# Kernel tuning notes

Hardware: AMD Instinct MI355X
Metric: run time of the kernel (lower is better)

Reference implementation:

```python
import jax, jax.numpy as jnp
import numpy as np

BN_EPS = 1e-5


def _conv1x1(x, W, b):
    # x: (B, Cin, H, W), W: (Cout, Cin), b: (Cout,)
    return jnp.einsum('bchw,oc->bohw', x, W) + b[None, :, None, None]


def _bn(x, gamma, beta, mean, var):
    # inference-mode BatchNorm2d with running stats
    inv = gamma / jnp.sqrt(var + BN_EPS)
    return x * inv[None, :, None, None] + (beta - mean * inv)[None, :, None, None]


def setup_inputs() -> dict:
    key = jax.random.key(0)
    ks = jax.random.split(key, 8)
    B, N, C, H, W = 4, 3, 256, 48, 48
    Ck = C // 2  # key/query/value channels (scale=2)
    s = 0.02
    return {
        'x': jax.random.normal(ks[0], (B, N, C, H, W), jnp.float32),
        # f_key / f_query (shared): conv1x1 + BN
        'Wk': jax.random.normal(ks[1], (Ck, C), jnp.float32) * s,
        'bk': jnp.zeros((Ck,), jnp.float32),
        'gk': jnp.ones((Ck,), jnp.float32),
        'betak': jnp.zeros((Ck,), jnp.float32),
        'mk': jnp.zeros((Ck,), jnp.float32),
        'vk': jnp.ones((Ck,), jnp.float32),
        # f_value
        'Wv': jax.random.normal(ks[2], (Ck, C), jnp.float32) * s,
        'bv': jnp.zeros((Ck,), jnp.float32),
        # f_out
        'Wo': jax.random.normal(ks[3], (C, Ck), jnp.float32) * s,
        'bo': jnp.zeros((C,), jnp.float32),
        # fuse_layer: in = 2*C, out = C
        'Wf': jax.random.normal(ks[4], (C, 2 * C), jnp.float32) * s,
        'bf': jnp.zeros((C,), jnp.float32),
    }


def reference(x, Wk, bk, gk, betak, mk, vk, Wv, bv, Wo, bo, Wf, bf):
    B, N, C, H, W = x.shape  # N == 3
    HW = H * W
    Ck = Wk.shape[0]
    scale = Ck ** (-0.5)

    # Precompute shared key/query and value features for all 3 views
    xf = x.reshape(B * N, C, H, W)
    k_all = _bn(_conv1x1(xf, Wk, bk), gk, betak, mk, vk).reshape(B, N, Ck, HW)
    v_all = _conv1x1(xf, Wv, bv).reshape(B, N, Ck, HW)

    outs = []
    attn_maps = []
    for i in range(3):  # fixed small structural loop over views
        adj_ids = [j for j in range(3) if j != i]
        ref = x[:, i]                          # (B, C, H, W)
        q = k_all[:, i].transpose(0, 2, 1)     # (B, HW, Ck)  f_query == f_key
        matching = jnp.zeros_like(ref)
        for j in adj_ids:
            sim = jnp.einsum('bqc,bck->bqk', q, k_all[:, j]) * scale  # (B, HW, HW)
            attn = jax.nn.softmax(sim, axis=-1)
            ctx = jnp.einsum('bqk,bck->bcq', attn, v_all[:, j])       # (B, Ck, HW)
            ctx = ctx.reshape(B, Ck, H, W)
            matching = matching + _conv1x1(ctx, Wo, bo)
            if i == 0:
                attn_maps.append(attn)
        fuse = _conv1x1(jnp.concatenate([ref, matching], axis=1), Wf, bf)
        outs.append(ref + fuse)

    out = jnp.stack(outs, axis=1)                    # (B, 3, C, H, W)
    attention_maps = jnp.stack(attn_maps, axis=1)    # (B, 2, HW, HW)
    return out, attention_maps
```

## Files before the change

kernel.cpp:

```cpp
#include <hip/hip_runtime.h>

typedef short s8v __attribute__((ext_vector_type(8)));
typedef short s4v __attribute__((ext_vector_type(4)));
typedef float f4v __attribute__((ext_vector_type(4)));
typedef unsigned u32v2 __attribute__((ext_vector_type(2)));
typedef unsigned short u16;

#define MFMA(a,b,c) __builtin_amdgcn_mfma_f32_16x16x32_bf16(a,b,c,0,0,0)

__device__ __forceinline__ float bf2f(u16 x){
  unsigned u = ((unsigned)x) << 16;
  return __builtin_bit_cast(float, u);
}
__device__ __forceinline__ u16 f2bf(float f){
  unsigned u = __builtin_bit_cast(unsigned, f);
  u += 0x7FFFu + ((u >> 16) & 1u);
  return (u16)(u >> 16);
}
__device__ __forceinline__ unsigned cvtpk(float lo, float hi){
  unsigned r;
  asm("v_cvt_pk_bf16_f32 %0, %1, %2" : "=v"(r) : "v"(lo), "v"(hi));
  return r;
}

__device__ __forceinline__ void gload16(const void* g, void* l){
  __builtin_amdgcn_global_load_lds((const __attribute__((address_space(1))) unsigned*)g,
                                   (__attribute__((address_space(3))) unsigned*)l, 16, 0, 0);
}
__device__ __forceinline__ void nt_store4(float* p, f4v v){
  __builtin_nontemporal_store(v, (f4v*)p);
}

#define CC   256
#define CK   128
#define HW   2304
#define NF   12
#define C2E  0.1275174996992022f
#define OFF_KT   0u
#define OFF_V    7077888u
#define OFF_CTX  14155776u
#define OFF_RS   42467328u
#define OFF_PAR  42909696u
#define OFF_WK16 42911744u
#define OFF_WV16 42977280u
#define OFF_WF16 43042816u
#define OFF_WCMB 43304960u

__global__ void k0_params(const float* __restrict__ Wkf, const float* __restrict__ Wvf,
                          const float* __restrict__ bk, const float* __restrict__ gk,
                          const float* __restrict__ betak, const float* __restrict__ mk,
                          const float* __restrict__ vk, const float* __restrict__ Wo,
                          const float* __restrict__ Wf, const float* __restrict__ bo,
                          const float* __restrict__ bfv,
                          u16* __restrict__ Wk16, u16* __restrict__ Wv16, u16* __restrict__ Wf16,
                          float* kscale, float* kbias, float* btot, u16* Wcomb){
  int c = blockIdx.x;
  int o = threadIdx.x;
  int gid = c*256 + o;
  Wk16[gid] = f2bf(Wkf[gid]);
  Wv16[gid] = f2bf(Wvf[gid]);
  {
    f4v wf4 = *(const f4v*)(Wf + (size_t)gid*4);
    #pragma unroll
    for(int u=0;u<4;u++) Wf16[(size_t)gid*4+u] = f2bf(wf4[u]);
  }
  float acc = 0.f;
  for(int m=0;m<256;m++)
    acc += Wf[(size_t)o*512 + 256 + m] * Wo[(size_t)m*128 + c];
  Wcomb[(size_t)o*128 + c] = f2bf(acc);
  if (c == 0){
    float a2 = 0.f;
    for(int m=0;m<256;m++)
      a2 += Wf[(size_t)o*512 + 256 + m] * bo[m];
    btot[o] = bfv[o] + 2.0f*a2;
    if (o < 128){
      float inv = gk[o] * rsqrtf(vk[o] + 1e-5f);
      kscale[o] = inv;
      kbias[o]  = betak[o] + (bk[o] - mk[o])*inv;
    }
  }
}

__device__ __forceinline__ void stage_xt(const float* __restrict__ xf, int pb, int tid, char* xt){
  #pragma unroll
  for(int it=0; it<8; ++it){
    int idx = tid + 256*it;
    int cp = idx>>4, slot = idx&15;
    const float* s0 = xf + (size_t)(2*cp  )*HW + pb + slot*4;
    const float* s1 = xf + (size_t)(2*cp+1)*HW + pb + slot*4;
    f4v va = *(const f4v*)s0;
    f4v vb = *(const f4v*)s1;
    #pragma unroll
    for(int u=0;u<4;u++){
      int p = slot*4+u;
      *(unsigned*)(xt + p*512 + ((4*cp) ^ ((p&7)<<4))) = cvtpk(va[u], vb[u]);
    }
  }
}
__device__ __forceinline__ s8v xt_frag(const char* xt, int r, int kt, int g){
  return *(const s8v*)(xt + r*512 + (((unsigned)(64*kt+16*g)) ^ ((unsigned)(r&7)<<4)));
}

__global__ __launch_bounds__(256) void k1_kv(const float* __restrict__ x, const u16* __restrict__ Wk,
                                             const u16* __restrict__ Wv, const float* __restrict__ bv,
                                             const float* __restrict__ kscale, const float* __restrict__ kbias,
                                             u16* __restrict__ kT, u16* __restrict__ vout){
  int f  = blockIdx.y;
  int pb = blockIdx.x*64;
  int tid = threadIdx.x;
  int w = tid>>6, l = tid&63, s = l&15, g = l>>4;
  __shared__ char xt[32768];
  stage_xt(x + (size_t)f*CC*HW, pb, tid, xt);
  __syncthreads();
  {
    s8v afr[8];
    #pragma unroll
    for(int kt=0;kt<8;kt++) afr[kt] = xt_frag(xt, 16*w+s, kt, g);
    f4v acc[8] = {};
    #pragma unroll
    for(int kt=0;kt<8;kt++){
      #pragma unroll
      for(int nt=0;nt<8;nt++){
        s8v b = *(const s8v*)(Wk + (size_t)(16*nt+s)*CC + 32*kt + 8*g);
        acc[nt] = MFMA(afr[kt], b, acc[nt]);
      }
    }
    u16* kout = kT + (size_t)f*HW*CK;
    int q0 = pb + 16*w;
    #pragma unroll
    for(int nt=0;nt<8;nt++){
      int o = 16*nt + s;
      float sc = kscale[o], bi = kbias[o];
      #pragma unroll
      for(int r=0;r<4;r++){
        int q = q0 + 4*g + r;
        kout[(size_t)q*CK + o] = f2bf(acc[nt][r]*sc + bi);
      }
    }
  }
  {
    s8v afr[2][8];
    #pragma unroll
    for(int mt=0;mt<2;mt++)
      #pragma unroll
      for(int kt=0;kt<8;kt++)
        afr[mt][kt] = *(const s8v*)(Wv + (size_t)(32*w+16*mt+s)*CC + 32*kt + 8*g);
    f4v acc[2][4] = {};
    #pragma unroll
    for(int kt=0;kt<8;kt++){
      #pragma unroll
      for(int nt=0;nt<4;nt++){
        s8v b = xt_frag(xt, 16*nt+s, kt, g);
        #pragma unroll
        for(int mt=0;mt<2;mt++)
          acc[mt][nt] = MFMA(afr[mt][kt], b, acc[mt][nt]);
      }
    }
    u16* vf = vout + (size_t)f*CK*HW;
    #pragma unroll
    for(int mt=0;mt<2;mt++){
      #pragma unroll
      for(int r=0;r<4;r++){
        int o = 32*w + 16*mt + 4*g + r;
        float bvo = bv[o];
        #pragma unroll
        for(int nt=0;nt<4;nt++)
          vf[(size_t)o*HW + pb + 16*nt + s] = f2bf(acc[mt][nt][r] + bvo);
      }
    }
  }
}

__global__ __launch_bounds__(256, 2) void k2_attn(const u16* __restrict__ kT, const u16* __restrict__ v,
                                                  u16* __restrict__ ctxS, float* __restrict__ rs){
  int qb  = blockIdx.x;
  int yy  = blockIdx.y;
  int bij = yy>>1, half = yy&1;
  int b = bij/6, r6_ = bij - 6*b, i = r6_>>1, jj = r6_&1;
  int adj0 = (i==0) ? 1 : 0;
  int adj1 = (i==2) ? 1 : 2;
  int j = jj ? adj1 : adj0;
  int tid = threadIdx.x;
  int w = tid>>6, l = tid&63, s = l&15, g = l>>4;
  int q0 = qb*128 + w*32;

  __shared__ char L[81920];
  char* plw = L + 65536 + w*4096;

  const u16* kTi = kT + (size_t)(b*3+i)*HW*CK;
  const u16* kTj = kT + (size_t)(b*3+j)*HW*CK;
  const u16* vj  = v  + (size_t)(b*3+j)*CK*HW;

  s8v qfr[2][4];
  #pragma unroll
  for(int qf=0;qf<2;qf++)
    #pragma unroll
    for(int kt=0;kt<4;kt++)
      qfr[qf][kt] = *(const s8v*)(kTi + (size_t)(q0+16*qf+s)*CK + 32*kt + 8*g);

  f4v ctx[8][2] = {};
  float psum[2] = {0.f, 0.f};

  auto STAGE = [&](int p0, int buf){
    const char* kbase = (const char*)kTj + (size_t)p0*256;
    const char* vbase = (const char*)vj  + (size_t)p0*2;
    char* lK = L + buf*16384 + w*1024;
    char* lV = L + 32768 + buf*16384 + w*1024;
    #pragma unroll
    for(int it=0; it<4; ++it){
      unsigned Lo = (unsigned)tid*16u + (unsigned)it*4096u;
      unsigned Gs = Lo ^ (((Lo>>8)&7u)<<4);
      gload16(kbase + Gs, lK + it*4096);
      unsigned row = Lo>>7;
      unsigned col = (Lo & 127u) ^ ((row&7u)<<4);
      gload16(vbase + (size_t)row*(HW*2) + col, lV + it*4096);
    }
  };

  int pbase = half*18;
  STAGE(pbase*64, 0);
  __syncthreads();
  int cur = 0;

  for(int pt=0; pt<18; ++pt){
    int p0 = (pbase + pt)*64;
    if (pt < 17) STAGE(p0+64, cur^1);
    const char* lK = L + cur*16384;
    const char* lV = L + 32768 + cur*16384;

    f4v sa[2][4] = {};
    #pragma unroll
    for(int kt=0;kt<4;kt++){
      #pragma unroll
      for(int nt=0;nt<4;nt++){
        unsigned row = (unsigned)(16*nt + s);
        unsigned cb  = ((unsigned)(64*kt + 16*g)) ^ ((row&7u)<<4);
        s8v kfr = *(const s8v*)(lK + row*256 + cb);
        #pragma unroll
        for(int qf=0;qf<2;qf++) sa[qf][nt] = MFMA(kfr, qfr[qf][kt], sa[qf][nt]);
      }
    }
    #pragma unroll
    for(int qf=0;qf<2;qf++){
      #pragma unroll
      for(int nt=0;nt<4;nt++){
        float e0 = exp2f(sa[qf][nt][0]*C2E);
        float e1 = exp2f(sa[qf][nt][1]*C2E);
        float e2 = exp2f(sa[qf][nt][2]*C2E);
        float e3 = exp2f(sa[qf][nt][3]*C2E);
        psum[qf] += (e0+e1)+(e2+e3);
        u32v2 pk;
        pk[0] = cvtpk(e0, e1);
        pk[1] = cvtpk(e2, e3);
        unsigned off = ((unsigned)(32*nt + 8*g)) ^ ((unsigned)(s&7)<<4);
        *(u32v2*)(plw + (unsigned)qf*2048u + (unsigned)s*128u + off) = pk;
      }
    }
    s8v pf[2][2];
    #pragma unroll
    for(int qf=0;qf<2;qf++)
      #pragma unroll
      for(int kt=0;kt<2;kt++)
        pf[qf][kt] = *(const s8v*)(plw + (unsigned)qf*2048u + (unsigned)s*128u +
                                   (((unsigned)(64*kt + 16*g)) ^ ((unsigned)(s&7)<<4)));
    #pragma unroll
    for(int kt=0;kt<2;kt++){
      #pragma unroll
      for(int ct=0;ct<8;ct++){
        unsigned row = (unsigned)(16*ct + s);
        unsigned cb  = ((unsigned)(64*kt + 16*g)) ^ ((row&7u)<<4);
        s8v vfr = *(const s8v*)(lV + row*128 + cb);
        #pragma unroll
        for(int qf=0;qf<2;qf++) ctx[ct][qf] = MFMA(vfr, pf[qf][kt], ctx[ct][qf]);
      }
    }
    __syncthreads();
    cur ^= 1;
  }

  #pragma unroll
  for(int qf=0;qf<2;qf++){
    float xsum = psum[qf];
    xsum += __shfl_xor(xsum, 16);
    xsum += __shfl_xor(xsum, 32);
    if (l < 16)
      rs[(size_t)yy*HW + q0 + 16*qf + s] = xsum;
  }
  u16* cS = ctxS + (size_t)yy*HW*CK;
  #pragma unroll
  for(int qf=0;qf<2;qf++){
    #pragma unroll
    for(int ct=0;ct<8;ct++){
      u32v2 pk;
      pk[0] = cvtpk(ctx[ct][qf][0], ctx[ct][qf][1]);
      pk[1] = cvtpk(ctx[ct][qf][2], ctx[ct][qf][3]);
      *(u32v2*)(cS + (size_t)(q0+16*qf+s)*CK + 16*ct + 4*g) = pk;
    }
  }
}

__global__ __launch_bounds__(256) void k2c_attnmap(const u16* __restrict__ kT,
                                                   const float* __restrict__ rs,
                                                   float* __restrict__ attn_out){
  int qb = blockIdx.x;
  int y  = blockIdx.y;
  int plane = y>>1, ph = y&1;
  int b = plane>>1, jj = plane&1, j = jj + 1;
  int tid = threadIdx.x;
  int w = tid>>6, l = tid&63, s = l&15, g = l>>4;
  int q0 = qb*64 + w*16;

  __shared__ char  ldsK[16384];
  __shared__ float ptile[4][16][68];
  __shared__ float inv16[4][16];

  const u16* kTi = kT + (size_t)(b*3)*HW*CK;
  const u16* kTj = kT + (size_t)(b*3+j)*HW*CK;

  s8v qf[4];
  #pragma unroll
  for(int kt=0;kt<4;kt++) qf[kt] = *(const s8v*)(kTi + (size_t)(q0+s)*CK + 32*kt + 8*g);

  {
    f4v ra = *(const f4v*)(rs + (size_t)(12*b+2*jj  )*HW + q0 + 4*g);
    f4v rb = *(const f4v*)(rs + (size_t)(12*b+2*jj+1)*HW + q0 + 4*g);
    if (s == 0){
      #pragma unroll
      for(int r=0;r<4;r++) inv16[w][4*g+r] = 1.0f / (ra[r] + rb[r]);
    }
  }
  __syncthreads();

  float* ao = attn_out + (size_t)plane*HW*HW;

  for(int pt=ph*18; pt<ph*18+18; ++pt){
    int p0 = pt*64;
    {
      const char* kbase = (const char*)kTj + (size_t)p0*256;
      char* lK = (char*)ldsK + w*1024;
      #pragma unroll
      for(int it=0; it<4; ++it){
        unsigned Lo = (unsigned)tid*16u + (unsigned)it*4096u;
        unsigned Gs = Lo ^ (((Lo>>8)&7u)<<4);
        gload16(kbase + Gs, lK + it*4096);
      }
    }
    __syncthreads();

    f4v sa[4] = {};
    #pragma unroll
    for(int kt=0;kt<4;kt++){
      #pragma unroll
      for(int nt=0;nt<4;nt++){
        unsigned row = (unsigned)(16*nt + s);
        unsigned cb  = ((unsigned)(64*kt + 16*g)) ^ ((row&7u)<<4);
        s8v bfr = *(const s8v*)((const char*)ldsK + row*256 + cb);
        sa[nt] = MFMA(qf[kt], bfr, sa[nt]);
      }
    }
    #pragma unroll
    for(int r=0;r<4;r++){
      #pragma unroll
      for(int nt=0;nt<4;nt++)
        ptile[w][4*g+r][16*nt+s] = exp2f(sa[nt][r]*C2E);
    }
    #pragma unroll
    for(int pass=0; pass<4; ++pass){
      int row = 4*pass + g;
      float inv = inv16[w][row];
      f4v val = *(const f4v*)&ptile[w][row][4*s];
      #pragma unroll
      for(int u=0;u<4;u++) val[u] *= inv;
      nt_store4(ao + (size_t)(q0+row)*HW + p0 + 4*s, val);
    }
    __syncthreads();
  }
}

__global__ __launch_bounds__(256) void k3_out(const float* __restrict__ x,
                                              const u16* __restrict__ Wf, const u16* __restrict__ Wcomb,
                                              const float* __restrict__ btot, const u16* __restrict__ ctxS,
                                              const float* __restrict__ rs,
                                              float* __restrict__ out){
  int f = blockIdx.y, pb = blockIdx.x*64;
  int tid = threadIdx.x;
  int w = tid>>6, l = tid&63, s = l&15, g = l>>4;
  __shared__ char xt[32768];
  const float* xf = x + (size_t)f*CC*HW;
  stage_xt(xf, pb, tid, xt);
  __syncthreads();
  f4v acc[4][4] = {};
  #pragma unroll
  for(int kt=0;kt<8;kt++){
    s8v bfr[4];
    #pragma unroll
    for(int nt=0;nt<4;nt++) bfr[nt] = xt_frag(xt, 16*nt+s, kt, g);
    #pragma unroll
    for(int mt=0;mt<4;mt++){
      s8v a = *(const s8v*)(Wf + (size_t)(64*w+16*mt+s)*512 + 32*kt + 8*g);
      #pragma unroll
      for(int nt=0;nt<4;nt++) acc[mt][nt] = MFMA(a, bfr[nt], acc[mt][nt]);
    }
  }
  #pragma unroll
  for(int jj=0;jj<2;jj++){
    const u16* cA = ctxS + (size_t)(4*f+2*jj  )*HW*CK;
    const u16* cB = ctxS + (size_t)(4*f+2*jj+1)*HW*CK;
    f4v acc2[4][4] = {};
    #pragma unroll
    for(int kt=0;kt<4;kt++){
      s8v b0[4], b1[4];
      #pragma unroll
      for(int nt=0;nt<4;nt++){
        b0[nt] = *(const s8v*)(cA + (size_t)(pb+16*nt+s)*CK + 32*kt + 8*g);
        b1[nt] = *(const s8v*)(cB + (size_t)(pb+16*nt+s)*CK + 32*kt + 8*g);
      }
      #pragma unroll
      for(int mt=0;mt<4;mt++){
        s8v a = *(const s8v*)(Wcomb + (size_t)(64*w+16*mt+s)*CK + 32*kt + 8*g);
        #pragma unroll
        for(int nt=0;nt<4;nt++){
          acc2[mt][nt] = MFMA(a, b0[nt], acc2[mt][nt]);
          acc2[mt][nt] = MFMA(a, b1[nt], acc2[mt][nt]);
        }
      }
    }
    const float* rA = rs + (size_t)(4*f+2*jj  )*HW;
    const float* rB = rs + (size_t)(4*f+2*jj+1)*HW;
    float invq[4];
    #pragma unroll
    for(int nt=0;nt<4;nt++){
      int q = pb + 16*nt + s;
      invq[nt] = 1.0f / (rA[q] + rB[q]);
    }
    #pragma unroll
    for(int mt=0;mt<4;mt++)
      #pragma unroll
      for(int nt=0;nt<4;nt++)
        #pragma unroll
        for(int r=0;r<4;r++) acc[mt][nt][r] += acc2[mt][nt][r]*invq[nt];
  }
  float* of = out + (size_t)f*CC*HW;
  #pragma unroll
  for(int mt=0;mt<4;mt++){
    #pragma unroll
    for(int r=0;r<4;r++){
      int o = 64*w + 16*mt + 4*g + r;
      float bb = btot[o];
      #pragma unroll
      for(int nt=0;nt<4;nt++){
        int p = pb + 16*nt + s;
        of[(size_t)o*HW + p] = acc[mt][nt][r] + bb + xf[(size_t)o*HW + p];
      }
    }
  }
}

extern "C" void kernel_launch(void* const* d_in, const int* in_sizes, int n_in,
                              void* d_out, int out_size, void* d_ws, size_t ws_size,
                              hipStream_t stream) {
  const float* x     = (const float*)d_in[0];
  const float* Wk    = (const float*)d_in[1];
  const float* bk    = (const float*)d_in[2];
  const float* gk    = (const float*)d_in[3];
  const float* betak = (const float*)d_in[4];
  const float* mk    = (const float*)d_in[5];
  const float* vk    = (const float*)d_in[6];
  const float* Wv    = (const float*)d_in[7];
  const float* bv    = (const float*)d_in[8];
  const float* Wo    = (const float*)d_in[9];
  const float* bo    = (const float*)d_in[10];
  const float* Wf    = (const float*)d_in[11];
  const float* bf    = (const float*)d_in[12];
  float* out = (float*)d_out;

  char* ws = (char*)d_ws;
  u16*   kT     = (u16*)(ws + OFF_KT);
  u16*   vv     = (u16*)(ws + OFF_V);
  u16*   ctxS   = (u16*)(ws + OFF_CTX);
  float* rs     = (float*)(ws + OFF_RS);
  float* kscale = (float*)(ws + OFF_PAR);
  float* kbias  = kscale + 128;
  float* btot   = kbias + 128;
  u16*   Wk16   = (u16*)(ws + OFF_WK16);
  u16*   Wv16   = (u16*)(ws + OFF_WV16);
  u16*   Wf16   = (u16*)(ws + OFF_WF16);
  u16*   Wcomb  = (u16*)(ws + OFF_WCMB);

  float* attn = out + (size_t)NF*CC*HW;

  k0_params<<<dim3(128), dim3(256), 0, stream>>>(Wk, Wv, bk, gk, betak, mk, vk, Wo, Wf, bo, bf,
                                                 Wk16, Wv16, Wf16, kscale, kbias, btot, Wcomb);
  k1_kv<<<dim3(36,12), dim3(256), 0, stream>>>(x, Wk16, Wv16, bv, kscale, kbias, kT, vv);
  k2_attn<<<dim3(18,48), dim3(256), 0, stream>>>(kT, vv, ctxS, rs);
  k2c_attnmap<<<dim3(36,16), dim3(256), 0, stream>>>(kT, rs, attn);
  k3_out<<<dim3(36,12), dim3(256), 0, stream>>>(x, Wf16, Wcomb, btot, ctxS, rs, out);
}
```

Baseline: 224.6 us.

## Switch attention kernel to 32x32x16 MFMA with in-register P via permlane swap

The attention kernel's QK^T and PV products move from 16x16x32 bf16 MFMAs to 32x32x16 MFMAs. The exponentiated scores are repacked into PV operand fragments in registers with v_permlane32_swap instead of a per-wave LDS round trip, which drops 16 KB of shared memory. This aims to cut LDS traffic and instruction count and to raise MFMA efficiency. The larger accumulators (16-float vectors) raise register pressure, and the operand layout mapping must be exactly right to stay correct.

```diff
diff --git a/kernel.cpp b/kernel.cpp
--- a/kernel.cpp
+++ b/kernel.cpp
@@ -3,10 +3,13 @@
 typedef short s8v __attribute__((ext_vector_type(8)));
 typedef short s4v __attribute__((ext_vector_type(4)));
 typedef float f4v __attribute__((ext_vector_type(4)));
+typedef float f16v __attribute__((ext_vector_type(16)));
 typedef unsigned u32v2 __attribute__((ext_vector_type(2)));
+typedef unsigned u32v4 __attribute__((ext_vector_type(4)));
 typedef unsigned short u16;
 
-#define MFMA(a,b,c) __builtin_amdgcn_mfma_f32_16x16x32_bf16(a,b,c,0,0,0)
+#define MFMA(a,b,c)   __builtin_amdgcn_mfma_f32_16x16x32_bf16(a,b,c,0,0,0)
+#define MFMA32(a,b,c) __builtin_amdgcn_mfma_f32_32x32x16_bf16(a,b,c,0,0,0)
 
 __device__ __forceinline__ float bf2f(u16 x){
   unsigned u = ((unsigned)x) << 16;
@@ -21,6 +24,9 @@
   unsigned r;
   asm("v_cvt_pk_bf16_f32 %0, %1, %2" : "=v"(r) : "v"(lo), "v"(hi));
   return r;
+}
+__device__ __forceinline__ void plswap(unsigned &x, unsigned &y){
+  asm volatile("v_permlane32_swap_b32 %0, %1" : "+v"(x), "+v"(y));
 }
 
 __device__ __forceinline__ void gload16(const void* g, void* l){
@@ -181,25 +187,23 @@
   int adj1 = (i==2) ? 1 : 2;
   int j = jj ? adj1 : adj0;
   int tid = threadIdx.x;
-  int w = tid>>6, l = tid&63, s = l&15, g = l>>4;
+  int w = tid>>6, l = tid&63;
+  int lq = l&31, hh = l>>5;
   int q0 = qb*128 + w*32;
 
-  __shared__ char L[81920];
-  char* plw = L + 65536 + w*4096;
+  __shared__ char L[65536];
 
   const u16* kTi = kT + (size_t)(b*3+i)*HW*CK;
   const u16* kTj = kT + (size_t)(b*3+j)*HW*CK;
   const u16* vj  = v  + (size_t)(b*3+j)*CK*HW;
 
-  s8v qfr[2][4];
-  #pragma unroll
-  for(int qf=0;qf<2;qf++)
-    #pragma unroll
-    for(int kt=0;kt<4;kt++)
-      qfr[qf][kt] = *(const s8v*)(kTi + (size_t)(q0+16*qf+s)*CK + 32*kt + 8*g);
-
-  f4v ctx[8][2] = {};
-  float psum[2] = {0.f, 0.f};
+  s8v qfr[8];
+  #pragma unroll
+  for(int st=0; st<8; ++st)
+    qfr[st] = *(const s8v*)(kTi + (size_t)(q0+lq)*CK + 16*st + 8*hh);
+
+  f16v ctx[4] = {};
+  float psum = 0.f;
 
   auto STAGE = [&](int p0, int buf){
     const char* kbase = (const char*)kTj + (size_t)p0*256;
@@ -228,73 +232,66 @@
     const char* lK = L + cur*16384;
     const char* lV = L + 32768 + cur*16384;
 
-    f4v sa[2][4] = {};
-    #pragma unroll
-    for(int kt=0;kt<4;kt++){
-      #pragma unroll
-      for(int nt=0;nt<4;nt++){
-        unsigned row = (unsigned)(16*nt + s);
-        unsigned cb  = ((unsigned)(64*kt + 16*g)) ^ ((row&7u)<<4);
-        s8v kfr = *(const s8v*)(lK + row*256 + cb);
-        #pragma unroll
-        for(int qf=0;qf<2;qf++) sa[qf][nt] = MFMA(kfr, qfr[qf][kt], sa[qf][nt]);
-      }
-    }
-    #pragma unroll
-    for(int qf=0;qf<2;qf++){
-      #pragma unroll
-      for(int nt=0;nt<4;nt++){
-        float e0 = exp2f(sa[qf][nt][0]*C2E);
-        float e1 = exp2f(sa[qf][nt][1]*C2E);
-        float e2 = exp2f(sa[qf][nt][2]*C2E);
-        float e3 = exp2f(sa[qf][nt][3]*C2E);
-        psum[qf] += (e0+e1)+(e2+e3);
-        u32v2 pk;
-        pk[0] = cvtpk(e0, e1);
-        pk[1] = cvtpk(e2, e3);
-        unsigned off = ((unsigned)(32*nt + 8*g)) ^ ((unsigned)(s&7)<<4);
-        *(u32v2*)(plw + (unsigned)qf*2048u + (unsigned)s*128u + off) = pk;
-      }
-    }
-    s8v pf[2][2];
-    #pragma unroll
-    for(int qf=0;qf<2;qf++)
-      #pragma unroll
-      for(int kt=0;kt<2;kt++)
-        pf[qf][kt] = *(const s8v*)(plw + (unsigned)qf*2048u + (unsigned)s*128u +
-                                   (((unsigned)(64*kt + 16*g)) ^ ((unsigned)(s&7)<<4)));
-    #pragma unroll
-    for(int kt=0;kt<2;kt++){
-      #pragma unroll
-      for(int ct=0;ct<8;ct++){
-        unsigned row = (unsigned)(16*ct + s);
-        unsigned cb  = ((unsigned)(64*kt + 16*g)) ^ ((row&7u)<<4);
-        s8v vfr = *(const s8v*)(lV + row*128 + cb);
-        #pragma unroll
-        for(int qf=0;qf<2;qf++) ctx[ct][qf] = MFMA(vfr, pf[qf][kt], ctx[ct][qf]);
+    f16v sa[2] = {};
+    #pragma unroll
+    for(int st=0; st<8; ++st){
+      #pragma unroll
+      for(int pb=0; pb<2; ++pb){
+        unsigned row = (unsigned)(32*pb + lq);
+        unsigned cb_ = ((unsigned)(32*st + 16*hh)) ^ ((row&7u)<<4);
+        s8v kfr = *(const s8v*)(lK + row*256 + cb_);
+        sa[pb] = MFMA32(kfr, qfr[st], sa[pb]);
+      }
+    }
+    #pragma unroll
+    for(int pb=0; pb<2; ++pb){
+      float e0 = exp2f(sa[pb][0]*C2E),  e1 = exp2f(sa[pb][1]*C2E);
+      float e2 = exp2f(sa[pb][2]*C2E),  e3 = exp2f(sa[pb][3]*C2E);
+      float e4 = exp2f(sa[pb][4]*C2E),  e5 = exp2f(sa[pb][5]*C2E);
+      float e6 = exp2f(sa[pb][6]*C2E),  e7 = exp2f(sa[pb][7]*C2E);
+      float e8 = exp2f(sa[pb][8]*C2E),  e9 = exp2f(sa[pb][9]*C2E);
+      float ea = exp2f(sa[pb][10]*C2E), eb = exp2f(sa[pb][11]*C2E);
+      float ec = exp2f(sa[pb][12]*C2E), ed = exp2f(sa[pb][13]*C2E);
+      float ee = exp2f(sa[pb][14]*C2E), ef = exp2f(sa[pb][15]*C2E);
+      psum += ((e0+e1)+(e2+e3)) + ((e4+e5)+(e6+e7)) +
+              ((e8+e9)+(ea+eb)) + ((ec+ed)+(ee+ef));
+      unsigned c0 = cvtpk(e0,e1), c1 = cvtpk(e2,e3), c2 = cvtpk(e4,e5), c3 = cvtpk(e6,e7);
+      unsigned c4 = cvtpk(e8,e9), c5 = cvtpk(ea,eb), c6 = cvtpk(ec,ed), c7 = cvtpk(ee,ef);
+      plswap(c0, c2); plswap(c1, c3);
+      plswap(c4, c6); plswap(c5, c7);
+      u32v4 w0 = {c0, c1, c2, c3};
+      u32v4 w1 = {c4, c5, c6, c7};
+      s8v pf0 = __builtin_bit_cast(s8v, w0);
+      s8v pf1 = __builtin_bit_cast(s8v, w1);
+      #pragma unroll
+      for(int cb=0; cb<4; ++cb){
+        unsigned row = (unsigned)(32*cb + lq);
+        unsigned swz = (row&7u)<<4;
+        unsigned off0 = ((unsigned)(64*pb      + 16*hh)) ^ swz;
+        unsigned off1 = ((unsigned)(64*pb + 32 + 16*hh)) ^ swz;
+        s8v vf0 = *(const s8v*)(lV + row*128 + off0);
+        s8v vf1 = *(const s8v*)(lV + row*128 + off1);
+        ctx[cb] = MFMA32(vf0, pf0, ctx[cb]);
+        ctx[cb] = MFMA32(vf1, pf1, ctx[cb]);
       }
     }
     __syncthreads();
     cur ^= 1;
   }
 
-  #pragma unroll
-  for(int qf=0;qf<2;qf++){
-    float xsum = psum[qf];
-    xsum += __shfl_xor(xsum, 16);
-    xsum += __shfl_xor(xsum, 32);
-    if (l < 16)
-      rs[(size_t)yy*HW + q0 + 16*qf + s] = xsum;
-  }
+  float xsum = psum + __shfl_xor(psum, 32);
+  if (l < 32)
+    rs[(size_t)yy*HW + q0 + lq] = xsum;
+
   u16* cS = ctxS + (size_t)yy*HW*CK;
   #pragma unroll
-  for(int qf=0;qf<2;qf++){
-    #pragma unroll
-    for(int ct=0;ct<8;ct++){
+  for(int cb=0; cb<4; ++cb){
+    #pragma unroll
+    for(int qd=0; qd<4; ++qd){
       u32v2 pk;
-      pk[0] = cvtpk(ctx[ct][qf][0], ctx[ct][qf][1]);
-      pk[1] = cvtpk(ctx[ct][qf][2], ctx[ct][qf][3]);
-      *(u32v2*)(cS + (size_t)(q0+16*qf+s)*CK + 16*ct + 4*g) = pk;
+      pk[0] = cvtpk(ctx[cb][4*qd+0], ctx[cb][4*qd+1]);
+      pk[1] = cvtpk(ctx[cb][4*qd+2], ctx[cb][4*qd+3]);
+      *(u32v2*)(cS + (size_t)(q0+lq)*CK + 32*cb + 8*qd + 4*hh) = pk;
     }
   }
 }
```

Result: faster. 218.6 us, median of 3 (-2.7%).
